# Performance work log

Hardware: AMD Instinct MI355X
Metric: run time of the kernel (lower is better)

The kernel has to match this reference:

```python
import jax, jax.numpy as jnp
import numpy as np
import math

B, T, D, K, KER, H = 2, 2048, 1024, 16, 7, 2048


def _decay_logit_init(k: int, dmin: float = 0.9, dmax: float = 0.999) -> np.ndarray:
    decays = np.exp(np.linspace(math.log(dmin), math.log(dmax), k))
    return (np.log(decays) - np.log1p(-decays)).astype(np.float32)


def setup_inputs() -> dict:
    key = jax.random.key(0)
    ks = jax.random.split(key, 12)
    s = 0.02
    return {
        "x": jax.random.normal(ks[0], (B, T, D), jnp.float32),
        "conv_w": jax.random.normal(ks[1], (D, KER), jnp.float32) * s,   # depthwise causal conv taps
        "gate_w": jax.random.normal(ks[2], (D, D), jnp.float32) * (D ** -0.5),
        "gate_b": jnp.zeros((D,), jnp.float32),
        "up_w": jax.random.normal(ks[3], (D, H), jnp.float32) * (D ** -0.5),
        "up_b": jnp.zeros((H,), jnp.float32),
        "down_w": jax.random.normal(ks[4], (H, D), jnp.float32) * (H ** -0.5),
        "down_b": jnp.zeros((D,), jnp.float32),
        "sin_w": jax.random.normal(ks[5], (D, K * D), jnp.float32) * (D ** -0.5),
        "sout_w": jax.random.normal(ks[6], (K * D, D), jnp.float32) * ((K * D) ** -0.5),
        "decay_logit": jnp.asarray(_decay_logit_init(K)),
        "gl_w": jax.random.normal(ks[7], (D, 1), jnp.float32) * (D ** -0.5),
        "gl_b": jnp.zeros((1,), jnp.float32),
    }


def _rmsnorm(x, eps=1e-6):
    return x * jax.lax.rsqrt(jnp.mean(x * x, axis=-1, keepdims=True) + eps)


def reference(x, conv_w, gate_w, gate_b, up_w, up_b, down_w, down_b,
              sin_w, sout_w, decay_logit, gl_w, gl_b):
    b, t, d = x.shape
    k_taps = conv_w.shape[1]
    nk = decay_logit.shape[0]

    u = _rmsnorm(x)  # (B,T,D)

    # --- local mixer: causal depthwise conv (zero history buffer) + sigmoid gate + SiLU MLP ---
    u_pad = jnp.pad(u, ((0, 0), (k_taps - 1, 0), (0, 0)))
    y = sum(conv_w[:, j] * u_pad[:, j:j + t, :] for j in range(k_taps))  # (B,T,D)
    g = jax.nn.sigmoid(u @ gate_w + gate_b)
    h = y * g
    local = jax.nn.silu(h @ up_w + up_b) @ down_w + down_b

    # --- state bank: K leaky integrators, s_t = a*s_{t-1} + (1-a)*z_t ---
    z = (u @ sin_w).reshape(b, t, nk, d)  # (B,T,K,D)
    a = jax.nn.sigmoid(decay_logit)[:, None]  # (K,1)

    def step(s, z_t):
        s = a * s + (1.0 - a) * z_t
        return s, s

    s0 = jnp.zeros((b, nk, d), x.dtype)
    _, S = jax.lax.scan(step, s0, jnp.swapaxes(z, 0, 1))  # (T,B,K,D)
    S = jnp.swapaxes(S, 0, 1).reshape(b, t, nk * d)
    long_path = S @ sout_w  # (B,T,D)

    # --- gate fusion + residual (memory table is empty at init -> mem term == 0) ---
    g_long = jax.nn.sigmoid(u @ gl_w + gl_b)  # (B,T,1)
    return x + local + g_long * long_path
```

## Files before the change

kernel.cpp:

```cpp
#include <hip/hip_runtime.h>
#include <cstdint>
#include <cstddef>

typedef __attribute__((ext_vector_type(8))) short short8;
typedef __attribute__((ext_vector_type(4))) float floatx4;

#define DEV static __device__ __forceinline__

DEV unsigned short f2bf(float f) {
  union { float f; uint32_t u; } v; v.f = f;
  uint32_t r = v.u + 0x7fffu + ((v.u >> 16) & 1u);
  return (unsigned short)(r >> 16);
}
DEV float bf2f(unsigned short h) {
  union { uint32_t u; float f; } v; v.u = ((uint32_t)h) << 16; return v.f;
}
DEV float sigmoidf_(float x) { return 1.f / (1.f + __expf(-x)); }

DEV void gld_lds16(const unsigned short* g, unsigned short* l) {
  __builtin_amdgcn_global_load_lds(
      (const __attribute__((address_space(1))) void*)g,
      (__attribute__((address_space(3))) void*)l, 16, 0, 0);
}

__global__ __launch_bounds__(256) void transpose_kernel(
    const float* __restrict__ W, unsigned short* __restrict__ Wt,
    int Kdim, int Ndim) {
  __shared__ float tile[32][33];
  const int n0 = blockIdx.x * 32;
  const int k0 = blockIdx.y * 32;
  const int tx = threadIdx.x & 31;
  const int ty = threadIdx.x >> 5;
#pragma unroll
  for (int r = 0; r < 32; r += 8)
    tile[ty + r][tx] = W[(size_t)(k0 + ty + r) * Ndim + n0 + tx];
  __syncthreads();
#pragma unroll
  for (int r = 0; r < 32; r += 8)
    Wt[(size_t)(n0 + ty + r) * Kdim + k0 + tx] = f2bf(tile[tx][ty + r]);
}

__global__ __launch_bounds__(256) void cast_kernel(
    const float* __restrict__ W, unsigned short* __restrict__ Wb) {
  const size_t i = (size_t)blockIdx.x * 256 + threadIdx.x;
  const float4 v = ((const float4*)W)[i];
  ushort4 o;
  o.x = f2bf(v.x); o.y = f2bf(v.y); o.z = f2bf(v.z); o.w = f2bf(v.w);
  ((ushort4*)Wb)[i] = o;
}

__global__ __launch_bounds__(256) void rmsnorm_kernel(
    const float* __restrict__ x, const float* __restrict__ gl_w,
    const float* __restrict__ gl_b, unsigned short* __restrict__ u,
    float* __restrict__ gl_logit) {
  const int row = blockIdx.x;
  const int tid = threadIdx.x;
  const float4 v = ((const float4*)(x + (size_t)row * 1024))[tid];
  float ss = v.x * v.x + v.y * v.y + v.z * v.z + v.w * v.w;
#pragma unroll
  for (int o = 32; o > 0; o >>= 1) ss += __shfl_down(ss, o, 64);
  __shared__ float red[4];
  if ((tid & 63) == 0) red[tid >> 6] = ss;
  __syncthreads();
  const float tot = red[0] + red[1] + red[2] + red[3];
  const float r = rsqrtf(tot * (1.f / 1024.f) + 1e-6f);
  const float ux = v.x * r, uy = v.y * r, uz = v.z * r, uw = v.w * r;
  ushort4 ub;
  ub.x = f2bf(ux); ub.y = f2bf(uy); ub.z = f2bf(uz); ub.w = f2bf(uw);
  ((ushort4*)(u + (size_t)row * 1024))[tid] = ub;
  const float4 w4 = ((const float4*)gl_w)[tid];
  float dot = ux * w4.x + uy * w4.y + uz * w4.z + uw * w4.w;
#pragma unroll
  for (int o = 32; o > 0; o >>= 1) dot += __shfl_down(dot, o, 64);
  __syncthreads();
  if ((tid & 63) == 0) red[tid >> 6] = dot;
  __syncthreads();
  if (tid == 0) gl_logit[row] = red[0] + red[1] + red[2] + red[3] + gl_b[0];
}

template <int EPI>
__global__ __launch_bounds__(256, 2) void gemm_bt(
    const unsigned short* __restrict__ A, const unsigned short* __restrict__ Bt,
    const float* __restrict__ bias, void* __restrict__ Cout, int Ndim, int Kdim) {
  __shared__ unsigned short As[128 * 32];
  __shared__ unsigned short Bs[128 * 32];
  const int tid = threadIdx.x;
  const int wave = tid >> 6;
  const int lane = tid & 63;
  const size_t row0 = (size_t)blockIdx.x * 128;
  const size_t col0 = (size_t)blockIdx.y * 128;

  const int srow = wave * 32 + (lane >> 2);
  const int kofs = (lane & 3) * 8;
  const unsigned short* pA0 = A + (row0 + srow) * (size_t)Kdim + kofs;
  const unsigned short* pA1 = A + (row0 + srow + 16) * (size_t)Kdim + kofs;
  const unsigned short* pB0 = Bt + (col0 + srow) * (size_t)Kdim + kofs;
  const unsigned short* pB1 = Bt + (col0 + srow + 16) * (size_t)Kdim + kofs;
  unsigned short* lA0 = &As[(wave * 2 + 0) * 512];
  unsigned short* lA1 = &As[(wave * 2 + 1) * 512];
  unsigned short* lB0 = &Bs[(wave * 2 + 0) * 512];
  unsigned short* lB1 = &Bs[(wave * 2 + 1) * 512];

  const int wm = (wave & 1) * 64;
  const int wn = (wave >> 1) * 64;
  const int lr = lane & 15;
  const int lq = lane >> 4;
  const int a_off = (wm + lr) * 32 + lq * 8;
  const int b_off = (wn + lr) * 32 + lq * 8;

  floatx4 acc[4][4];
#pragma unroll
  for (int i = 0; i < 4; i++)
#pragma unroll
    for (int j = 0; j < 4; j++) acc[i][j] = floatx4{0.f, 0.f, 0.f, 0.f};

  for (int kt = 0; kt < Kdim; kt += 32) {
    __syncthreads();
    gld_lds16(pA0, lA0);
    gld_lds16(pA1, lA1);
    gld_lds16(pB0, lB0);
    gld_lds16(pB1, lB1);
    pA0 += 32; pA1 += 32; pB0 += 32; pB1 += 32;
    __syncthreads();
    short8 af[4], bfr[4];
#pragma unroll
    for (int i = 0; i < 4; i++) af[i] = *(const short8*)&As[a_off + i * 16 * 32];
#pragma unroll
    for (int j = 0; j < 4; j++) bfr[j] = *(const short8*)&Bs[b_off + j * 16 * 32];
#pragma unroll
    for (int i = 0; i < 4; i++)
#pragma unroll
      for (int j = 0; j < 4; j++)
        acc[i][j] = __builtin_amdgcn_mfma_f32_16x16x32_bf16(af[i], bfr[j], acc[i][j], 0, 0, 0);
  }

#pragma unroll
  for (int i = 0; i < 4; i++) {
    const size_t rbase = row0 + wm + 16 * i + lq * 4;
#pragma unroll
    for (int j = 0; j < 4; j++) {
      const size_t c = col0 + wn + 16 * j + lr;
#pragma unroll
      for (int r = 0; r < 4; r++) {
        float v = acc[i][j][r];
        const size_t off = (rbase + r) * (size_t)Ndim + c;
        if constexpr (EPI == 0) {
          ((unsigned short*)Cout)[off] = f2bf(v);
        } else if constexpr (EPI == 1) {
          v += bias[c];
          ((unsigned short*)Cout)[off] = f2bf(sigmoidf_(v));
        } else if constexpr (EPI == 2) {
          v += bias[c];
          ((unsigned short*)Cout)[off] = f2bf(v * sigmoidf_(v));
        } else {
          ((float*)Cout)[off] = v + bias[c];
        }
      }
    }
  }
}

__global__ __launch_bounds__(256, 2) void gemm_mt(
    const unsigned short* __restrict__ OT, const unsigned short* __restrict__ SB,
    unsigned short* __restrict__ MT) {
  __shared__ unsigned short As[128 * 32];
  __shared__ unsigned short Bs[128 * 32];
  const int kb = blockIdx.z;
  const int tid = threadIdx.x;
  const int wave = tid >> 6;
  const int lane = tid & 63;
  const size_t row0 = (size_t)blockIdx.x * 128;
  const size_t col0 = (size_t)blockIdx.y * 128;
  const size_t ld = 16384;

  const int srow = wave * 32 + (lane >> 2);
  const int kofs = (lane & 3) * 8;
  const unsigned short* pA0 = OT + (row0 + srow) * ld + kb * 1024 + kofs;
  const unsigned short* pA1 = OT + (row0 + srow + 16) * ld + kb * 1024 + kofs;
  const unsigned short* pB0 = SB + (col0 + srow) * ld + kb * 1024 + kofs;
  const unsigned short* pB1 = SB + (col0 + srow + 16) * ld + kb * 1024 + kofs;
  unsigned short* lA0 = &As[(wave * 2 + 0) * 512];
  unsigned short* lA1 = &As[(wave * 2 + 1) * 512];
  unsigned short* lB0 = &Bs[(wave * 2 + 0) * 512];
  unsigned short* lB1 = &Bs[(wave * 2 + 1) * 512];

  const int wm = (wave & 1) * 64;
  const int wn = (wave >> 1) * 64;
  const int lr = lane & 15;
  const int lq = lane >> 4;
  const int a_off = (wm + lr) * 32 + lq * 8;
  const int b_off = (wn + lr) * 32 + lq * 8;

  floatx4 acc[4][4];
#pragma unroll
  for (int i = 0; i < 4; i++)
#pragma unroll
    for (int j = 0; j < 4; j++) acc[i][j] = floatx4{0.f, 0.f, 0.f, 0.f};

  for (int kt = 0; kt < 1024; kt += 32) {
    __syncthreads();
    gld_lds16(pA0, lA0);
    gld_lds16(pA1, lA1);
    gld_lds16(pB0, lB0);
    gld_lds16(pB1, lB1);
    pA0 += 32; pA1 += 32; pB0 += 32; pB1 += 32;
    __syncthreads();
    short8 af[4], bfr[4];
#pragma unroll
    for (int i = 0; i < 4; i++) af[i] = *(const short8*)&As[a_off + i * 16 * 32];
#pragma unroll
    for (int j = 0; j < 4; j++) bfr[j] = *(const short8*)&Bs[b_off + j * 16 * 32];
#pragma unroll
    for (int i = 0; i < 4; i++)
#pragma unroll
      for (int j = 0; j < 4; j++)
        acc[i][j] = __builtin_amdgcn_mfma_f32_16x16x32_bf16(af[i], bfr[j], acc[i][j], 0, 0, 0);
  }

#pragma unroll
  for (int i = 0; i < 4; i++) {
    const size_t rbase = row0 + wm + 16 * i + lq * 4;
#pragma unroll
    for (int j = 0; j < 4; j++) {
      const size_t c = col0 + wn + 16 * j + lr;
#pragma unroll
      for (int r = 0; r < 4; r++)
        MT[(rbase + r) * ld + kb * 1024 + c] = f2bf(acc[i][j][r]);
    }
  }
}

__global__ __launch_bounds__(256, 2) void gemm_splitk(
    const unsigned short* __restrict__ A, const unsigned short* __restrict__ Bt,
    unsigned short* __restrict__ p0, unsigned short* __restrict__ p1,
    unsigned short* __restrict__ p2, int Ndim, int Kdim) {
  __shared__ unsigned short As[128 * 32];
  __shared__ unsigned short Bs[128 * 32];
  const int split = blockIdx.z;
  const int k0 = split * 5472;
  const int klen = (split == 2) ? 5440 : 5472;
  const int tid = threadIdx.x;
  const int wave = tid >> 6;
  const int lane = tid & 63;
  const size_t row0 = (size_t)blockIdx.x * 128;
  const size_t col0 = (size_t)blockIdx.y * 128;

  const int srow = wave * 32 + (lane >> 2);
  const int kofs = (lane & 3) * 8;
  const unsigned short* pA0 = A + (row0 + srow) * (size_t)Kdim + k0 + kofs;
  const unsigned short* pA1 = A + (row0 + srow + 16) * (size_t)Kdim + k0 + kofs;
  const unsigned short* pB0 = Bt + (col0 + srow) * (size_t)Kdim + k0 + kofs;
  const unsigned short* pB1 = Bt + (col0 + srow + 16) * (size_t)Kdim + k0 + kofs;
  unsigned short* lA0 = &As[(wave * 2 + 0) * 512];
  unsigned short* lA1 = &As[(wave * 2 + 1) * 512];
  unsigned short* lB0 = &Bs[(wave * 2 + 0) * 512];
  unsigned short* lB1 = &Bs[(wave * 2 + 1) * 512];

  const int wm = (wave & 1) * 64;
  const int wn = (wave >> 1) * 64;
  const int lr = lane & 15;
  const int lq = lane >> 4;
  const int a_off = (wm + lr) * 32 + lq * 8;
  const int b_off = (wn + lr) * 32 + lq * 8;

  floatx4 acc[4][4];
#pragma unroll
  for (int i = 0; i < 4; i++)
#pragma unroll
    for (int j = 0; j < 4; j++) acc[i][j] = floatx4{0.f, 0.f, 0.f, 0.f};

  for (int kt = 0; kt < klen; kt += 32) {
    __syncthreads();
    gld_lds16(pA0, lA0);
    gld_lds16(pA1, lA1);
    gld_lds16(pB0, lB0);
    gld_lds16(pB1, lB1);
    pA0 += 32; pA1 += 32; pB0 += 32; pB1 += 32;
    __syncthreads();
    short8 af[4], bfr[4];
#pragma unroll
    for (int i = 0; i < 4; i++) af[i] = *(const short8*)&As[a_off + i * 16 * 32];
#pragma unroll
    for (int j = 0; j < 4; j++) bfr[j] = *(const short8*)&Bs[b_off + j * 16 * 32];
#pragma unroll
    for (int i = 0; i < 4; i++)
#pragma unroll
      for (int j = 0; j < 4; j++)
        acc[i][j] = __builtin_amdgcn_mfma_f32_16x16x32_bf16(af[i], bfr[j], acc[i][j], 0, 0, 0);
  }

  unsigned short* P = (split == 0) ? p0 : (split == 1) ? p1 : p2;
#pragma unroll
  for (int i = 0; i < 4; i++) {
    const size_t rbase = row0 + wm + 16 * i + lq * 4;
#pragma unroll
    for (int j = 0; j < 4; j++) {
      const size_t c = col0 + wn + 16 * j + lr;
#pragma unroll
      for (int r = 0; r < 4; r++)
        P[(rbase + r) * (size_t)Ndim + c] = f2bf(acc[i][j][r]);
    }
  }
}

__global__ __launch_bounds__(256) void convgate_kernel(
    const unsigned short* __restrict__ u, const float* __restrict__ conv_w,
    const unsigned short* __restrict__ g, unsigned short* __restrict__ h) {
  const size_t idx = (size_t)blockIdx.x * 256 + threadIdx.x;
  const int d = (int)(idx & 1023);
  const int t = (int)((idx >> 10) & 2047);
  const unsigned short* up = u + idx;
  float acc = 0.f;
#pragma unroll
  for (int j = 0; j < 7; ++j) {
    const int tt = t - 6 + j;
    if (tt >= 0) acc += conv_w[d * 7 + j] * bf2f(up[(j - 6) * 1024]);
  }
  h[idx] = f2bf(acc * bf2f(g[idx]));
}

__global__ __launch_bounds__(256) void scan1u_kernel(
    const unsigned short* __restrict__ u, const float* __restrict__ decay_logit,
    float* __restrict__ carry) {
  const int gid = blockIdx.x * 256 + threadIdx.x;
  const int d = gid & 1023;
  const int b = (gid >> 10) & 1;
  const int c = gid >> 11;
  float a[16], s[16];
#pragma unroll
  for (int k = 0; k < 16; ++k) { a[k] = sigmoidf_(decay_logit[k]); s[k] = 0.f; }
  const unsigned short* p = u + ((size_t)b * 2048 + c * 128) * 1024 + d;
#pragma unroll 2
  for (int t = 0; t < 128; ++t) {
    const float uv = bf2f(*p);
    p += 1024;
#pragma unroll
    for (int k = 0; k < 16; ++k) s[k] = fmaf(a[k], s[k], (1.f - a[k]) * uv);
  }
#pragma unroll
  for (int k = 0; k < 16; ++k)
    carry[(size_t)((c * 2 + b) * 16 + k) * 1024 + d] = s[k];
}

__global__ __launch_bounds__(256) void scan2u_kernel(
    float* __restrict__ carry, const float* __restrict__ decay_logit) {
  const int gid = blockIdx.x * 256 + threadIdx.x;
  const int d = gid & 1023;
  const int k = (gid >> 10) & 15;
  const int b = gid >> 14;
  const float a = sigmoidf_(decay_logit[k]);
  float aL = a;
#pragma unroll
  for (int i = 0; i < 7; ++i) aL *= aL;
  float s = 0.f;
#pragma unroll
  for (int c = 0; c < 16; ++c) {
    const size_t idx = (size_t)((c * 2 + b) * 16 + k) * 1024 + d;
    const float Lc = carry[idx];
    carry[idx] = s;
    s = fmaf(aL, s, Lc);
  }
}

__global__ __launch_bounds__(256) void scan3u_kernel(
    const unsigned short* __restrict__ u, const float* __restrict__ decay_logit,
    const float* __restrict__ carry, unsigned short* __restrict__ Ucat) {
  const int gid = blockIdx.x * 256 + threadIdx.x;
  const int d = gid & 1023;
  const int k = (gid >> 10) & 15;
  const int b = (gid >> 14) & 1;
  const int c = gid >> 15;
  const float a = sigmoidf_(decay_logit[k]);
  const float na = 1.f - a;
  float s = carry[(size_t)((c * 2 + b) * 16 + k) * 1024 + d];
  const unsigned short* p = u + ((size_t)b * 2048 + c * 128) * 1024 + d;
  unsigned short* q = Ucat + ((size_t)b * 2048 + c * 128) * 16384 + k * 1024 + d;
#pragma unroll 4
  for (int t = 0; t < 128; ++t) {
    s = fmaf(a, s, na * bf2f(*p));
    *q = f2bf(s);
    p += 1024;
    q += 16384;
  }
}

__global__ __launch_bounds__(256) void fold_kernel(
    const float* __restrict__ x, const float* __restrict__ loc,
    float* __restrict__ out) {
  const size_t idx = (size_t)blockIdx.x * 256 + threadIdx.x;
  out[idx] = x[idx] + loc[idx];
}

__global__ __launch_bounds__(256) void reduce_kernel(
    const unsigned short* __restrict__ p0, const unsigned short* __restrict__ p1,
    const unsigned short* __restrict__ p2, const float* __restrict__ gl,
    float* __restrict__ out) {
  const size_t idx = (size_t)blockIdx.x * 256 + threadIdx.x;
  const float g = sigmoidf_(gl[idx >> 10]);
  const float sum = bf2f(p0[idx]) + bf2f(p1[idx]) + bf2f(p2[idx]);
  out[idx] += g * sum;
}

extern "C" void kernel_launch(void* const* d_in, const int* in_sizes, int n_in,
                              void* d_out, int out_size, void* d_ws,
                              size_t ws_size, hipStream_t stream) {
  const float* x      = (const float*)d_in[0];
  const float* conv_w = (const float*)d_in[1];
  const float* gate_w = (const float*)d_in[2];
  const float* gate_b = (const float*)d_in[3];
  const float* up_w   = (const float*)d_in[4];
  const float* up_b   = (const float*)d_in[5];
  const float* down_w = (const float*)d_in[6];
  const float* down_b = (const float*)d_in[7];
  const float* sin_w  = (const float*)d_in[8];
  const float* sout_w = (const float*)d_in[9];
  const float* decay  = (const float*)d_in[10];
  const float* gl_w   = (const float*)d_in[11];
  const float* gl_b   = (const float*)d_in[12];
  float* out = (float*)d_out;
  char* ws = (char*)d_ws;

  auto Ucat = (unsigned short*)(ws + ((size_t)0 << 20));
  auto GWT  = (unsigned short*)(ws + ((size_t)0 << 20));
  auto G    = (unsigned short*)(ws + ((size_t)2 << 20));
  auto Hb   = (unsigned short*)(ws + ((size_t)10 << 20));
  auto UWT  = (unsigned short*)(ws + ((size_t)18 << 20));
  auto Mb   = (unsigned short*)(ws + ((size_t)22 << 20));
  auto DWT  = (unsigned short*)(ws + ((size_t)38 << 20));
  auto SB   = (unsigned short*)(ws + ((size_t)0 << 20));
  auto OT   = (unsigned short*)(ws + ((size_t)32 << 20));
  auto LOC  = (float*)(ws + ((size_t)128 << 20));
  auto MT   = (unsigned short*)(ws + ((size_t)128 << 20));
  auto U    = (unsigned short*)(ws + ((size_t)160 << 20));
  auto P2   = (unsigned short*)(ws + ((size_t)160 << 20));
  auto CARRY= (float*)(ws + ((size_t)168 << 20));
  auto P0   = (unsigned short*)(ws + ((size_t)168 << 20));
  auto P1   = (unsigned short*)(ws + ((size_t)176 << 20));
  auto GL   = (float*)(ws + ((size_t)184 << 20));

  rmsnorm_kernel<<<4096, 256, 0, stream>>>(x, gl_w, gl_b, U, GL);

  transpose_kernel<<<dim3(32, 32), 256, 0, stream>>>(gate_w, GWT, 1024, 1024);
  gemm_bt<1><<<dim3(32, 8), 256, 0, stream>>>(U, GWT, gate_b, G, 1024, 1024);
  convgate_kernel<<<16384, 256, 0, stream>>>(U, conv_w, G, Hb);
  transpose_kernel<<<dim3(64, 32), 256, 0, stream>>>(up_w, UWT, 1024, 2048);
  gemm_bt<2><<<dim3(32, 16), 256, 0, stream>>>(Hb, UWT, up_b, Mb, 2048, 1024);
  transpose_kernel<<<dim3(32, 64), 256, 0, stream>>>(down_w, DWT, 2048, 1024);
  gemm_bt<3><<<dim3(32, 8), 256, 0, stream>>>(Mb, DWT, down_b, LOC, 1024, 2048);
  fold_kernel<<<16384, 256, 0, stream>>>(x, LOC, out);

  cast_kernel<<<16384, 256, 0, stream>>>(sin_w, SB);
  transpose_kernel<<<dim3(32, 512), 256, 0, stream>>>(sout_w, OT, 16384, 1024);
  gemm_mt<<<dim3(8, 8, 16), 256, 0, stream>>>(OT, SB, MT);

  scan1u_kernel<<<128, 256, 0, stream>>>(U, decay, CARRY);
  scan2u_kernel<<<128, 256, 0, stream>>>(CARRY, decay);
  scan3u_kernel<<<2048, 256, 0, stream>>>(U, decay, CARRY, Ucat);

  gemm_splitk<<<dim3(32, 8, 3), 256, 0, stream>>>(Ucat, MT, P0, P1, P2, 1024, 16384);
  reduce_kernel<<<16384, 256, 0, stream>>>(P0, P1, P2, GL, out);
}
```

Baseline: 613.3 us.

## Replace split-K partial buffers with atomic fp32 accumulation and raise split counts

Adds a split-K GEMM that accumulates fp32 results with atomicAdd straight into the destination. The gate and down GEMMs now use 2 and 4 K-splits to fill more CUs, with the bias and sigmoid moved into the conv and fold kernels. The long-path GEMM writes gated results directly into the output with 6 splits, which removes the bf16 partial buffers and the reduce kernel. In exchange it adds memsets, atomic traffic contention and non-deterministic summation order.

```diff
diff --git a/kernel.cpp b/kernel.cpp
--- a/kernel.cpp
+++ b/kernel.cpp
@@ -144,16 +144,91 @@
       for (int r = 0; r < 4; r++) {
         float v = acc[i][j][r];
         const size_t off = (rbase + r) * (size_t)Ndim + c;
-        if constexpr (EPI == 0) {
-          ((unsigned short*)Cout)[off] = f2bf(v);
-        } else if constexpr (EPI == 1) {
-          v += bias[c];
-          ((unsigned short*)Cout)[off] = f2bf(sigmoidf_(v));
-        } else if constexpr (EPI == 2) {
+        if constexpr (EPI == 2) {
           v += bias[c];
           ((unsigned short*)Cout)[off] = f2bf(v * sigmoidf_(v));
         } else {
-          ((float*)Cout)[off] = v + bias[c];
+          ((unsigned short*)Cout)[off] = f2bf(v);
+        }
+      }
+    }
+  }
+}
+
+template <int EPI>
+__global__ __launch_bounds__(256, 2) void gemm_atomic(
+    const unsigned short* __restrict__ A, const unsigned short* __restrict__ Bt,
+    float* __restrict__ Cacc, int Ndim, int Kdim, int splitLen,
+    const float* __restrict__ gl) {
+  __shared__ unsigned short As[128 * 32];
+  __shared__ unsigned short Bs[128 * 32];
+  const int k0 = blockIdx.z * splitLen;
+  const int klen = min(splitLen, Kdim - k0);
+  const int tid = threadIdx.x;
+  const int wave = tid >> 6;
+  const int lane = tid & 63;
+  const size_t row0 = (size_t)blockIdx.x * 128;
+  const size_t col0 = (size_t)blockIdx.y * 128;
+
+  const int srow = wave * 32 + (lane >> 2);
+  const int kofs = (lane & 3) * 8;
+  const unsigned short* pA0 = A + (row0 + srow) * (size_t)Kdim + k0 + kofs;
+  const unsigned short* pA1 = A + (row0 + srow + 16) * (size_t)Kdim + k0 + kofs;
+  const unsigned short* pB0 = Bt + (col0 + srow) * (size_t)Kdim + k0 + kofs;
+  const unsigned short* pB1 = Bt + (col0 + srow + 16) * (size_t)Kdim + k0 + kofs;
+  unsigned short* lA0 = &As[(wave * 2 + 0) * 512];
+  unsigned short* lA1 = &As[(wave * 2 + 1) * 512];
+  unsigned short* lB0 = &Bs[(wave * 2 + 0) * 512];
+  unsigned short* lB1 = &Bs[(wave * 2 + 1) * 512];
+
+  const int wm = (wave & 1) * 64;
+  const int wn = (wave >> 1) * 64;
+  const int lr = lane & 15;
+  const int lq = lane >> 4;
+  const int a_off = (wm + lr) * 32 + lq * 8;
+  const int b_off = (wn + lr) * 32 + lq * 8;
+
+  floatx4 acc[4][4];
+#pragma unroll
+  for (int i = 0; i < 4; i++)
+#pragma unroll
+    for (int j = 0; j < 4; j++) acc[i][j] = floatx4{0.f, 0.f, 0.f, 0.f};
+
+  for (int kt = 0; kt < klen; kt += 32) {
+    __syncthreads();
+    gld_lds16(pA0, lA0);
+    gld_lds16(pA1, lA1);
+    gld_lds16(pB0, lB0);
+    gld_lds16(pB1, lB1);
+    pA0 += 32; pA1 += 32; pB0 += 32; pB1 += 32;
+    __syncthreads();
+    short8 af[4], bfr[4];
+#pragma unroll
+    for (int i = 0; i < 4; i++) af[i] = *(const short8*)&As[a_off + i * 16 * 32];
+#pragma unroll
+    for (int j = 0; j < 4; j++) bfr[j] = *(const short8*)&Bs[b_off + j * 16 * 32];
+#pragma unroll
+    for (int i = 0; i < 4; i++)
+#pragma unroll
+      for (int j = 0; j < 4; j++)
+        acc[i][j] = __builtin_amdgcn_mfma_f32_16x16x32_bf16(af[i], bfr[j], acc[i][j], 0, 0, 0);
+  }
+
+#pragma unroll
+  for (int i = 0; i < 4; i++) {
+    const size_t rbase = row0 + wm + 16 * i + lq * 4;
+#pragma unroll
+    for (int j = 0; j < 4; j++) {
+      const size_t c = col0 + wn + 16 * j + lr;
+#pragma unroll
+      for (int r = 0; r < 4; r++) {
+        const size_t row = rbase + r;
+        const size_t off = row * (size_t)Ndim + c;
+        if constexpr (EPI == 0) {
+          atomicAdd(&Cacc[off], acc[i][j][r]);
+        } else {
+          const float g = sigmoidf_(gl[row]);
+          atomicAdd(&Cacc[off], g * acc[i][j][r]);
         }
       }
     }
@@ -230,82 +305,10 @@
   }
 }
 
-__global__ __launch_bounds__(256, 2) void gemm_splitk(
-    const unsigned short* __restrict__ A, const unsigned short* __restrict__ Bt,
-    unsigned short* __restrict__ p0, unsigned short* __restrict__ p1,
-    unsigned short* __restrict__ p2, int Ndim, int Kdim) {
-  __shared__ unsigned short As[128 * 32];
-  __shared__ unsigned short Bs[128 * 32];
-  const int split = blockIdx.z;
-  const int k0 = split * 5472;
-  const int klen = (split == 2) ? 5440 : 5472;
-  const int tid = threadIdx.x;
-  const int wave = tid >> 6;
-  const int lane = tid & 63;
-  const size_t row0 = (size_t)blockIdx.x * 128;
-  const size_t col0 = (size_t)blockIdx.y * 128;
-
-  const int srow = wave * 32 + (lane >> 2);
-  const int kofs = (lane & 3) * 8;
-  const unsigned short* pA0 = A + (row0 + srow) * (size_t)Kdim + k0 + kofs;
-  const unsigned short* pA1 = A + (row0 + srow + 16) * (size_t)Kdim + k0 + kofs;
-  const unsigned short* pB0 = Bt + (col0 + srow) * (size_t)Kdim + k0 + kofs;
-  const unsigned short* pB1 = Bt + (col0 + srow + 16) * (size_t)Kdim + k0 + kofs;
-  unsigned short* lA0 = &As[(wave * 2 + 0) * 512];
-  unsigned short* lA1 = &As[(wave * 2 + 1) * 512];
-  unsigned short* lB0 = &Bs[(wave * 2 + 0) * 512];
-  unsigned short* lB1 = &Bs[(wave * 2 + 1) * 512];
-
-  const int wm = (wave & 1) * 64;
-  const int wn = (wave >> 1) * 64;
-  const int lr = lane & 15;
-  const int lq = lane >> 4;
-  const int a_off = (wm + lr) * 32 + lq * 8;
-  const int b_off = (wn + lr) * 32 + lq * 8;
-
-  floatx4 acc[4][4];
-#pragma unroll
-  for (int i = 0; i < 4; i++)
-#pragma unroll
-    for (int j = 0; j < 4; j++) acc[i][j] = floatx4{0.f, 0.f, 0.f, 0.f};
-
-  for (int kt = 0; kt < klen; kt += 32) {
-    __syncthreads();
-    gld_lds16(pA0, lA0);
-    gld_lds16(pA1, lA1);
-    gld_lds16(pB0, lB0);
-    gld_lds16(pB1, lB1);
-    pA0 += 32; pA1 += 32; pB0 += 32; pB1 += 32;
-    __syncthreads();
-    short8 af[4], bfr[4];
-#pragma unroll
-    for (int i = 0; i < 4; i++) af[i] = *(const short8*)&As[a_off + i * 16 * 32];
-#pragma unroll
-    for (int j = 0; j < 4; j++) bfr[j] = *(const short8*)&Bs[b_off + j * 16 * 32];
-#pragma unroll
-    for (int i = 0; i < 4; i++)
-#pragma unroll
-      for (int j = 0; j < 4; j++)
-        acc[i][j] = __builtin_amdgcn_mfma_f32_16x16x32_bf16(af[i], bfr[j], acc[i][j], 0, 0, 0);
-  }
-
-  unsigned short* P = (split == 0) ? p0 : (split == 1) ? p1 : p2;
-#pragma unroll
-  for (int i = 0; i < 4; i++) {
-    const size_t rbase = row0 + wm + 16 * i + lq * 4;
-#pragma unroll
-    for (int j = 0; j < 4; j++) {
-      const size_t c = col0 + wn + 16 * j + lr;
-#pragma unroll
-      for (int r = 0; r < 4; r++)
-        P[(rbase + r) * (size_t)Ndim + c] = f2bf(acc[i][j][r]);
-    }
-  }
-}
-
-__global__ __launch_bounds__(256) void convgate_kernel(
+__global__ __launch_bounds__(256) void sigconv_kernel(
     const unsigned short* __restrict__ u, const float* __restrict__ conv_w,
-    const unsigned short* __restrict__ g, unsigned short* __restrict__ h) {
+    const float* __restrict__ gacc, const float* __restrict__ gate_b,
+    unsigned short* __restrict__ h) {
   const size_t idx = (size_t)blockIdx.x * 256 + threadIdx.x;
   const int d = (int)(idx & 1023);
   const int t = (int)((idx >> 10) & 2047);
@@ -316,7 +319,8 @@
     const int tt = t - 6 + j;
     if (tt >= 0) acc += conv_w[d * 7 + j] * bf2f(up[(j - 6) * 1024]);
   }
-  h[idx] = f2bf(acc * bf2f(g[idx]));
+  const float g = sigmoidf_(gacc[idx] + gate_b[d]);
+  h[idx] = f2bf(acc * g);
 }
 
 __global__ __launch_bounds__(256) void scan1u_kernel(
@@ -386,19 +390,9 @@
 
 __global__ __launch_bounds__(256) void fold_kernel(
     const float* __restrict__ x, const float* __restrict__ loc,
-    float* __restrict__ out) {
+    const float* __restrict__ down_b, float* __restrict__ out) {
   const size_t idx = (size_t)blockIdx.x * 256 + threadIdx.x;
-  out[idx] = x[idx] + loc[idx];
-}
-
-__global__ __launch_bounds__(256) void reduce_kernel(
-    const unsigned short* __restrict__ p0, const unsigned short* __restrict__ p1,
-    const unsigned short* __restrict__ p2, const float* __restrict__ gl,
-    float* __restrict__ out) {
-  const size_t idx = (size_t)blockIdx.x * 256 + threadIdx.x;
-  const float g = sigmoidf_(gl[idx >> 10]);
-  const float sum = bf2f(p0[idx]) + bf2f(p1[idx]) + bf2f(p2[idx]);
-  out[idx] += g * sum;
+  out[idx] = x[idx] + loc[idx] + down_b[idx & 1023];
 }
 
 extern "C" void kernel_launch(void* const* d_in, const int* in_sizes, int n_in,
@@ -422,32 +416,33 @@
 
   auto Ucat = (unsigned short*)(ws + ((size_t)0 << 20));
   auto GWT  = (unsigned short*)(ws + ((size_t)0 << 20));
-  auto G    = (unsigned short*)(ws + ((size_t)2 << 20));
   auto Hb   = (unsigned short*)(ws + ((size_t)10 << 20));
   auto UWT  = (unsigned short*)(ws + ((size_t)18 << 20));
   auto Mb   = (unsigned short*)(ws + ((size_t)22 << 20));
   auto DWT  = (unsigned short*)(ws + ((size_t)38 << 20));
   auto SB   = (unsigned short*)(ws + ((size_t)0 << 20));
   auto OT   = (unsigned short*)(ws + ((size_t)32 << 20));
-  auto LOC  = (float*)(ws + ((size_t)128 << 20));
+  auto GACC = (float*)(ws + ((size_t)128 << 20));
+  auto LOC  = (float*)(ws + ((size_t)144 << 20));
   auto MT   = (unsigned short*)(ws + ((size_t)128 << 20));
   auto U    = (unsigned short*)(ws + ((size_t)160 << 20));
-  auto P2   = (unsigned short*)(ws + ((size_t)160 << 20));
   auto CARRY= (float*)(ws + ((size_t)168 << 20));
-  auto P0   = (unsigned short*)(ws + ((size_t)168 << 20));
-  auto P1   = (unsigned short*)(ws + ((size_t)176 << 20));
-  auto GL   = (float*)(ws + ((size_t)184 << 20));
+  auto GL   = (float*)(ws + ((size_t)170 << 20));
 
   rmsnorm_kernel<<<4096, 256, 0, stream>>>(x, gl_w, gl_b, U, GL);
 
+  hipMemsetAsync(GACC, 0, (size_t)16 << 20, stream);
   transpose_kernel<<<dim3(32, 32), 256, 0, stream>>>(gate_w, GWT, 1024, 1024);
-  gemm_bt<1><<<dim3(32, 8), 256, 0, stream>>>(U, GWT, gate_b, G, 1024, 1024);
-  convgate_kernel<<<16384, 256, 0, stream>>>(U, conv_w, G, Hb);
+  gemm_atomic<0><<<dim3(32, 8, 2), 256, 0, stream>>>(U, GWT, GACC, 1024, 1024,
+                                                     512, nullptr);
+  sigconv_kernel<<<16384, 256, 0, stream>>>(U, conv_w, GACC, gate_b, Hb);
   transpose_kernel<<<dim3(64, 32), 256, 0, stream>>>(up_w, UWT, 1024, 2048);
   gemm_bt<2><<<dim3(32, 16), 256, 0, stream>>>(Hb, UWT, up_b, Mb, 2048, 1024);
+  hipMemsetAsync(LOC, 0, (size_t)16 << 20, stream);
   transpose_kernel<<<dim3(32, 64), 256, 0, stream>>>(down_w, DWT, 2048, 1024);
-  gemm_bt<3><<<dim3(32, 8), 256, 0, stream>>>(Mb, DWT, down_b, LOC, 1024, 2048);
-  fold_kernel<<<16384, 256, 0, stream>>>(x, LOC, out);
+  gemm_atomic<0><<<dim3(32, 8, 4), 256, 0, stream>>>(Mb, DWT, LOC, 1024, 2048,
+                                                     512, nullptr);
+  fold_kernel<<<16384, 256, 0, stream>>>(x, LOC, down_b, out);
 
   cast_kernel<<<16384, 256, 0, stream>>>(sin_w, SB);
   transpose_kernel<<<dim3(32, 512), 256, 0, stream>>>(sout_w, OT, 16384, 1024);
@@ -457,6 +452,6 @@
   scan2u_kernel<<<128, 256, 0, stream>>>(CARRY, decay);
   scan3u_kernel<<<2048, 256, 0, stream>>>(U, decay, CARRY, Ucat);
 
-  gemm_splitk<<<dim3(32, 8, 3), 256, 0, stream>>>(Ucat, MT, P0, P1, P2, 1024, 16384);
-  reduce_kernel<<<16384, 256, 0, stream>>>(P0, P1, P2, GL, out);
-}
+  gemm_atomic<1><<<dim3(32, 8, 6), 256, 0, stream>>>(Ucat, MT, out, 1024, 16384,
+                                                     2752, GL);
+}
```

Measured after the change: 709.2 us. 15.6% more time.
